# Optimization experiments

Measured on AMD Instinct MI355X. Metric: run time of the kernel, lower is better.

Reference implementation:

```python
import jax, jax.numpy as jnp
import numpy as np

NUM_EMBEDDINGS = 8192
EMBEDDING_DIM = 512
COMMITMENT_COST = 0.25


def setup_inputs() -> dict:
    key = jax.random.key(0)
    kz, ke = jax.random.split(key)
    z = jax.random.normal(kz, (2, EMBEDDING_DIM, 8, 32, 32), dtype=jnp.float32)
    # matches nn.Embedding init uniform_(-1/K, 1/K)
    emb_w = jax.random.uniform(
        ke, (NUM_EMBEDDINGS, EMBEDDING_DIM), dtype=jnp.float32,
        minval=-1.0 / NUM_EMBEDDINGS, maxval=1.0 / NUM_EMBEDDINGS)
    return {"z": z, "emb_w": emb_w}


def reference(z, emb_w):
    B, C, F, H, W = z.shape
    # [B,C,F,H,W] -> [N, C]
    z_flat = jnp.transpose(z, (0, 2, 3, 4, 1)).reshape(-1, C)
    # squared L2 distances via expansion: |z|^2 + |e|^2 - 2 z.e
    dist = (jnp.sum(z_flat * z_flat, axis=1, keepdims=True)
            + jnp.sum(emb_w * emb_w, axis=1)
            - 2.0 * jnp.matmul(z_flat, emb_w.T))  # [N, K]
    indices = jnp.argmin(dist, axis=1)  # [N]
    z_q_flat = emb_w[indices]  # [N, C]
    z_q = jnp.transpose(z_q_flat.reshape(B, F, H, W, C), (0, 4, 1, 2, 3))
    diff = z_q - z
    mse = jnp.mean(diff * diff)
    # codebook_loss == commitment_loss numerically (detach only affects grads)
    vq_loss = mse + COMMITMENT_COST * mse
    # straight-through estimator: value equals z_q
    z_q_ste = z + jax.lax.stop_gradient(z_q - z)
    indices = indices.reshape(B, F, H, W)
    return (z_q_ste, vq_loss, indices)
```

## Files before the change

### kernel.cpp

```cpp
#include <hip/hip_runtime.h>


constexpr int KCB = 8192;
constexpr int CD  = 512;
constexpr int SD  = 8192;
constexpr int NB  = 2;
constexpr int NR  = NB * SD;
constexpr long ZQ_ELEMS = (long)NB * CD * SD;

constexpr size_t WS_CNT   = 64;
constexpr size_t WS_KEYS  = 128;
constexpr size_t WS_RISK  = 139264;
constexpr size_t WS_IDX   = 212992;
constexpr size_t WS_LIST  = 286720;
constexpr size_t WS_ZNORM = 360448;
constexpr size_t WS_ENORM = 425984;
constexpr size_t WS_EMBT  = 458752;
constexpr size_t WS_ZH    = 17235968;
constexpr size_t WS_ZM    = 34013184;
constexpr size_t WS_EH    = 50790400;
constexpr size_t WS_EM    = 59179008;

#define RISK_EPS 2.0e-7f
#define WINDOW   1.3e-4f

constexpr int BUFB = 50176;

typedef __attribute__((ext_vector_type(8))) short short8;
typedef __attribute__((ext_vector_type(4))) float f32x4;

__device__ __forceinline__ unsigned int fkey(float f) {
  unsigned int b = __float_as_uint(f);
  return (b & 0x80000000u) ? ~b : (b | 0x80000000u);
}
__device__ __forceinline__ float unfkey(unsigned int u) {
  return (u & 0x80000000u) ? __uint_as_float(u ^ 0x80000000u)
                           : __uint_as_float(~u);
}
__device__ __forceinline__ ushort bf16_rne(float f, float* back) {
  unsigned int u = __float_as_uint(f);
  ushort h = (ushort)((u + 0x7FFFu + ((u >> 16) & 1u)) >> 16);
  *back = __uint_as_float((unsigned int)h << 16);
  return h;
}
__device__ __forceinline__ void gload16(const void* g, void* l) {
  __builtin_amdgcn_global_load_lds(
      (const __attribute__((address_space(1))) unsigned int*)g,
      (__attribute__((address_space(3))) unsigned int*)l, 16, 0, 0);
}

__global__ __launch_bounds__(256) void k_znorm(const float* __restrict__ z,
                                               float* __restrict__ znorm) {
  int n0 = blockIdx.x * 256;
  int b = n0 / SD, s0 = n0 % SD;
  const float* zp = z + (size_t)b * CD * SD + s0 + threadIdx.x;
  double a = 0.0;
  #pragma unroll 8
  for (int c = 0; c < CD; ++c) {
    double v = (double)zp[(size_t)c * SD];
    a = fma(v, v, a);
  }
  znorm[n0 + threadIdx.x] = (float)a;
}

__global__ __launch_bounds__(256) void k_enorm(const float* __restrict__ emb,
                                               float* __restrict__ enorm) {
  int row  = blockIdx.x * 4 + (threadIdx.x >> 6);
  int lane = threadIdx.x & 63;
  const float4* p = (const float4*)(emb + (size_t)row * CD);
  float4 a = p[lane * 2], b = p[lane * 2 + 1];
  float s = a.x*a.x + a.y*a.y + a.z*a.z + a.w*a.w
          + b.x*b.x + b.y*b.y + b.z*b.z + b.w*b.w;
  #pragma unroll
  for (int off = 32; off; off >>= 1) s += __shfl_down(s, off);
  if (lane == 0) enorm[row] = s;
}

__global__ __launch_bounds__(256) void k_transpose(const float* __restrict__ emb,
                                                   float* __restrict__ embt) {
  __shared__ float t[64][65];
  int bk = blockIdx.x & 127, bc = blockIdx.x >> 7;
  int k0 = bk * 64, c0 = bc * 64;
  int t4 = threadIdx.x & 15, tq = threadIdx.x >> 4;
  #pragma unroll
  for (int p = 0; p < 4; ++p) {
    int kk = p * 16 + tq;
    float4 v = *(const float4*)(emb + (size_t)(k0 + kk) * CD + c0 + 4 * t4);
    t[kk][4*t4+0] = v.x; t[kk][4*t4+1] = v.y; t[kk][4*t4+2] = v.z; t[kk][4*t4+3] = v.w;
  }
  __syncthreads();
  #pragma unroll
  for (int p = 0; p < 4; ++p) {
    int cc = p * 16 + tq;
    float4 v;
    v.x = t[4*t4+0][cc]; v.y = t[4*t4+1][cc]; v.z = t[4*t4+2][cc]; v.w = t[4*t4+3][cc];
    *(float4*)(embt + (size_t)(c0 + cc) * KCB + k0 + 4 * t4) = v;
  }
}


__global__ __launch_bounds__(256) void k_zsplit(const float* __restrict__ z,
                                                ushort* __restrict__ zh,
                                                ushort* __restrict__ zm) {
  __shared__ float t[32][257];
  int rt = blockIdx.x >> 4, ct = blockIdx.x & 15;
  int n0 = rt * 256;
  int b = n0 >> 13, s0 = n0 & (SD - 1);
  const float* zp = z + (size_t)b * CD * SD + (size_t)(ct * 32) * SD + s0;
  #pragma unroll 4
  for (int c = 0; c < 32; ++c)
    t[c][threadIdx.x] = zp[(size_t)c * SD + threadIdx.x];
  __syncthreads();
  size_t tbase = ((size_t)rt * 16 + ct) * 8192;
  #pragma unroll
  for (int p = 0; p < 4; ++p) {
    int slot = p * 256 + threadIdx.x;
    int r = slot >> 2, cs = slot & 3;
    int csw = cs ^ ((r >> 1) & 3);
    union { ushort u[8]; int4 v; } ph, pm;
    #pragma unroll
    for (int j = 0; j < 8; ++j) {
      float f = t[cs * 8 + j][r];
      float fh, fm;
      ph.u[j] = bf16_rne(f, &fh);
      float r1 = f - fh;
      pm.u[j] = bf16_rne(r1, &fm);
    }
    size_t off = tbase + (size_t)r * 32 + csw * 8;
    *(int4*)(zh + off) = ph.v;
    *(int4*)(zm + off) = pm.v;
  }
}

__global__ __launch_bounds__(256) void k_esplit(const float* __restrict__ emb,
                                                ushort* __restrict__ eh,
                                                ushort* __restrict__ em) {
  __shared__ float t[32][257];
  int rt = blockIdx.x >> 4, ct = blockIdx.x & 15;
  int k0 = rt * 256;
  #pragma unroll 4
  for (int i = 0; i < 32; ++i) {
    int idx = i * 256 + threadIdx.x;
    int r = idx >> 5, c = idx & 31;
    t[c][r] = emb[(size_t)(k0 + r) * CD + ct * 32 + c];
  }
  __syncthreads();
  size_t tbase = ((size_t)rt * 16 + ct) * 8192;
  #pragma unroll
  for (int p = 0; p < 4; ++p) {
    int slot = p * 256 + threadIdx.x;
    int r = slot >> 2, cs = slot & 3;
    int csw = cs ^ ((r >> 1) & 3);
    union { ushort u[8]; int4 v; } ph, pm;
    #pragma unroll
    for (int j = 0; j < 8; ++j) {
      float f = t[cs * 8 + j][r];
      float fh, fm;
      ph.u[j] = bf16_rne(f, &fh);
      float r1 = f - fh;
      pm.u[j] = bf16_rne(r1, &fm);
    }
    size_t off = tbase + (size_t)r * 32 + csw * 8;
    *(int4*)(eh + off) = ph.v;
    *(int4*)(em + off) = pm.v;
  }
}

__global__ __launch_bounds__(512, 2) void k_dist_mfma(
    const ushort* __restrict__ zh, const ushort* __restrict__ zm,
    const ushort* __restrict__ eh, const ushort* __restrict__ em,
    const float* __restrict__ enorm_g, const float* __restrict__ znorm,
    unsigned long long* __restrict__ keys, unsigned int* __restrict__ riskArr) {
  extern __shared__ __align__(16) char smem[];

  int tid  = threadIdx.x;
  int lane = tid & 63;
  int wid  = tid >> 6;
  int wm = wid >> 2, wn = wid & 3;
  int lk = lane >> 4, lc = lane & 15;

  int bid = (int)blockIdx.x;
  int swz = (bid & 7) * 32 + (bid >> 3);
  int m0    = (swz >> 1) * 128;
  int khalf = swz & 1;
  int n_rt  = m0 >> 8;
  int ahalf = (m0 >> 7) & 1;

  size_t thr8  = (size_t)tid * 8;
  int    tid16 = tid * 16;
  int    lane16 = lane * 16;

  int afo[4], bfo[4];
  #pragma unroll
  for (int mi = 0; mi < 4; ++mi) {
    int rowA = wm * 64 + mi * 16 + lc;
    afo[mi] = rowA * 64 + ((lk ^ ((rowA >> 1) & 3)) << 4);
  }
  #pragma unroll
  for (int ni = 0; ni < 4; ++ni) {
    int rowB = wn * 64 + ni * 16 + lc;
    bfo[ni] = rowB * 64 + ((lk ^ ((rowB >> 1) & 3)) << 4);
  }

  float Aab[16];
  #pragma unroll
  for (int li = 0; li < 16; ++li)
    Aab[li] = znorm[m0 + wm * 64 + (li >> 2) * 16 + lk * 4 + (li & 3)];

  unsigned long long bkey[16];
  float rminv[16];
  #pragma unroll
  for (int li = 0; li < 16; ++li) { bkey[li] = ~0ull; rminv[li] = 3.402823466e38f; }

#define STAGE(s_) do {                                                   \
    int it_ = (s_) >> 4, ks_ = (s_) & 15;                                \
    char* lb_ = smem + ((s_) % 3) * BUFB;                                \
    size_t ae_ = (size_t)(n_rt * 16 + ks_) * 8192 + (size_t)ahalf * 4096 \
                 + thr8;                                                 \
    size_t be_ = (size_t)((khalf * 16 + it_) * 16 + ks_) * 8192 + thr8;  \
    gload16(zh + ae_,        lb_ + tid16);                               \
    gload16(zm + ae_,        lb_ + 8192 + tid16);                        \
    gload16(eh + be_,        lb_ + 16384 + tid16);                       \
    gload16(eh + be_ + 4096, lb_ + 24576 + tid16);                       \
    gload16(em + be_,        lb_ + 32768 + tid16);                       \
    gload16(em + be_ + 4096, lb_ + 40960 + tid16);                       \
    gload16(enorm_g + (size_t)(khalf * 4096 + it_ * 256) + lane * 4,     \
            lb_ + 49152 + lane16);                                       \
  } while (0)

  STAGE(0);
  STAGE(1);

  for (int it = 0; it < 16; ++it) {
    f32x4 acc[4][4];
    #pragma unroll
    for (int mi = 0; mi < 4; ++mi)
      #pragma unroll
      for (int ni = 0; ni < 4; ++ni) {
        f32x4 zz = {0.f, 0.f, 0.f, 0.f};
        acc[mi][ni] = zz;
      }

    for (int ks = 0; ks < 16; ++ks) {
      int s = it * 16 + ks;
      if (s + 2 < 256) asm volatile("s_waitcnt vmcnt(7)" ::: "memory");
      else             asm volatile("s_waitcnt vmcnt(0)" ::: "memory");
      __builtin_amdgcn_s_barrier();
      __builtin_amdgcn_sched_barrier(0);
      if (s + 2 < 256) STAGE(s + 2);

      const char* Cb = smem + (s % 3) * BUFB;
      short8 a_h[4], a_m[4];
      #pragma unroll
      for (int mi = 0; mi < 4; ++mi) {
        a_h[mi] = *(const short8*)(Cb + afo[mi]);
        a_m[mi] = *(const short8*)(Cb + 8192 + afo[mi]);
      }
      #pragma unroll
      for (int ni = 0; ni < 4; ++ni) {
        short8 b_h = *(const short8*)(Cb + 16384 + bfo[ni]);
        short8 b_m = *(const short8*)(Cb + 32768 + bfo[ni]);
        #pragma unroll
        for (int mi = 0; mi < 4; ++mi)
          acc[mi][ni] = __builtin_amdgcn_mfma_f32_16x16x32_bf16(a_h[mi], b_h, acc[mi][ni], 0, 0, 0);
        #pragma unroll
        for (int mi = 0; mi < 4; ++mi)
          acc[mi][ni] = __builtin_amdgcn_mfma_f32_16x16x32_bf16(a_h[mi], b_m, acc[mi][ni], 0, 0, 0);
        #pragma unroll
        for (int mi = 0; mi < 4; ++mi)
          acc[mi][ni] = __builtin_amdgcn_mfma_f32_16x16x32_bf16(a_m[mi], b_h, acc[mi][ni], 0, 0, 0);
      }
    }

    int N0 = khalf * 4096 + it * 256;
    const char* Eb = smem + ((it * 16 + 15) % 3) * BUFB + 49152;
    #pragma unroll
    for (int ni = 0; ni < 4; ++ni) {
      int coff = wn * 64 + ni * 16 + lc;
      int col = N0 + coff;
      float en = *(const float*)(Eb + coff * 4);
      #pragma unroll
      for (int mi = 0; mi < 4; ++mi) {
        #pragma unroll
        for (int r = 0; r < 4; ++r) {
          int li = mi * 4 + r;
          float ab = Aab[li] + en;
          float q  = -2.0f * acc[mi][ni][r];
          float sv = ab + q;
          float bvv = sv - ab;
          float t   = q - bvv;
          unsigned int su = __float_as_uint(sv);
          float ulp = __uint_as_float(su & 0x7f800000u) * 1.1920929e-7f;
          bool risky = (0.5f * ulp - fabsf(t)) < RISK_EPS;
          if (((su & 0x7fffffu) == 0u) && (t < 0.f))
            risky |= ((0.25f * ulp + t) < RISK_EPS);
          unsigned long long key =
              ((unsigned long long)fkey(sv) << 32) | (unsigned int)col;
          if (key < bkey[li]) bkey[li] = key;
          if (risky && sv < rminv[li]) rminv[li] = sv;
        }
      }
    }
  }
#undef STAGE

  __syncthreads();
  unsigned long long* red = (unsigned long long*)smem;
  #pragma unroll
  for (int li = 0; li < 16; ++li) {
    int row = wm * 64 + (li >> 2) * 16 + lk * 4 + (li & 3);
    red[row * 64 + wn * 16 + lc] = bkey[li];
  }
  __syncthreads();
  if (tid < 128) {
    unsigned long long mn = ~0ull;
    #pragma unroll 4
    for (int i = 0; i < 64; ++i) {
      unsigned long long v = red[tid * 64 + i];
      if (v < mn) mn = v;
    }
    atomicMin(&keys[m0 + tid], mn);
  }
  __syncthreads();
  unsigned int* red2 = (unsigned int*)smem;
  #pragma unroll
  for (int li = 0; li < 16; ++li) {
    int row = wm * 64 + (li >> 2) * 16 + lk * 4 + (li & 3);
    red2[row * 64 + wn * 16 + lc] = fkey(rminv[li]);
  }
  __syncthreads();
  if (tid < 128) {
    unsigned int mn = 0xFFFFFFFFu;
    #pragma unroll 4
    for (int i = 0; i < 64; ++i) {
      unsigned int v = red2[tid * 64 + i];
      if (v < mn) mn = v;
    }
    atomicMin(&riskArr[m0 + tid], mn);
  }
}

__global__ __launch_bounds__(256) void k_resolve(const unsigned long long* __restrict__ keys,
                                                 const unsigned int* __restrict__ riskArr,
                                                 int* __restrict__ idxArr,
                                                 int* __restrict__ list,
                                                 unsigned int* __restrict__ cnt) {
  int row = blockIdx.x * 256 + threadIdx.x;
  unsigned long long kk = keys[row];
  idxArr[row] = (int)(kk & 0xffffffffull) & (KCB - 1);
  float smin = unfkey((unsigned int)(kk >> 32));
  float rmin = unfkey(riskArr[row]);
  if (rmin <= smin + WINDOW) {
    unsigned int pos = atomicAdd(cnt, 1u);
    list[pos & (NR - 1)] = row;
  }
}

__global__ __launch_bounds__(256) void k_rescan(const float* __restrict__ z,
                                                const float* __restrict__ embt,
                                                const float* __restrict__ enorm,
                                                const float* __restrict__ znorm,
                                                const int* __restrict__ list,
                                                const unsigned int* __restrict__ cnt,
                                                int* __restrict__ idxArr) {
  __shared__ float zs[512];
  __shared__ unsigned long long rk[256];
  int tid = threadIdx.x;
  unsigned int nr = *cnt;
  if (nr > (unsigned int)NR) nr = NR;
  for (unsigned int li = blockIdx.x; li < nr; li += gridDim.x) {
    int row = list[li] & (NR - 1);
    int b = row >> 13, s = row & (SD - 1);
    const float* zp = z + (size_t)b * CD * SD + s;
    zs[tid]       = zp[(size_t)tid * SD];
    zs[tid + 256] = zp[(size_t)(tid + 256) * SD];
    __syncthreads();
    float A = znorm[row];
    unsigned long long best = ~0ull;
    #pragma unroll 1
    for (int g = 0; g < 8; ++g) {
      int ka = tid + g * 1024;
      float a0 = 0.f, a1 = 0.f, a2 = 0.f, a3 = 0.f;
      #pragma unroll 8
      for (int c = 0; c < CD; ++c) {
        const float* ep = embt + (size_t)c * KCB + ka;
        float zc = zs[c];
        a0 = fmaf(zc, ep[0],   a0);
        a1 = fmaf(zc, ep[256], a1);
        a2 = fmaf(zc, ep[512], a2);
        a3 = fmaf(zc, ep[768], a3);
      }
      float av[4] = {a0, a1, a2, a3};
      #pragma unroll
      for (int jj = 0; jj < 4; ++jj) {
        int k = ka + jj * 256;
        float d = (A + enorm[k]) - 2.0f * av[jj];
        unsigned long long key =
            ((unsigned long long)fkey(d) << 32) | (unsigned int)k;
        if (key < best) best = key;
      }
    }
    rk[tid] = best;
    __syncthreads();
    for (int s2 = 128; s2; s2 >>= 1) {
      if (tid < s2 && rk[tid + s2] < rk[tid]) rk[tid] = rk[tid + s2];
      __syncthreads();
    }
    if (tid == 0) idxArr[row] = (int)(rk[0] & 0xffffffffull) & (KCB - 1);
    __syncthreads();
  }
}

__global__ __launch_bounds__(256) void k_gather(const float* __restrict__ z,
                                                const float* __restrict__ emb,
                                                const int* __restrict__ idxArr,
                                                float* __restrict__ out,
                                                double* __restrict__ acc) {
  __shared__ float q[64][129];
  __shared__ int   idxs[64];
  __shared__ float wpart[4];
  int tid = threadIdx.x;
  int n0 = blockIdx.x * 64;
  int b = n0 >> 13, s0 = n0 & (SD - 1);
  if (tid < 64) {
    int idx = idxArr[n0 + tid] & (KCB - 1);
    idxs[tid] = idx;
    out[ZQ_ELEMS + 1 + n0 + tid] = (float)idx;
  }
  __syncthreads();
  int sl = tid & 63;
  int cg = tid >> 6;
  float sum = 0.f;
  const float* zb = z   + (size_t)b * CD * SD + s0 + sl;
  float*       ob = out + (size_t)b * CD * SD + s0 + sl;
  for (int cc = 0; cc < 4; ++cc) {
    int cbase = cc * 128;
    __syncthreads();
    {
      int r = tid >> 2, p = tid & 3;
      const float* e = emb + (size_t)idxs[r] * CD + cbase + p * 32;
      #pragma unroll
      for (int j = 0; j < 8; ++j) {
        float4 v = *(const float4*)(e + j * 4);
        q[r][p*32 + j*4 + 0] = v.x; q[r][p*32 + j*4 + 1] = v.y;
        q[r][p*32 + j*4 + 2] = v.z; q[r][p*32 + j*4 + 3] = v.w;
      }
    }
    __syncthreads();
    #pragma unroll 8
    for (int j = 0; j < 32; ++j) {
      int c = cbase + cg * 32 + j;
      float zv = zb[(size_t)c * SD];
      float qv = q[sl][cg * 32 + j];
      float d = qv - zv;
      sum += d * d;
      ob[(size_t)c * SD] = zv + (qv - zv);
    }
  }
  #pragma unroll
  for (int off = 32; off; off >>= 1) sum += __shfl_down(sum, off);
  if ((tid & 63) == 0) wpart[tid >> 6] = sum;
  __syncthreads();
  if (tid == 0) {
    double t = (double)wpart[0] + (double)wpart[1] + (double)wpart[2] + (double)wpart[3];
    atomicAdd(acc, t);
  }
}

__global__ void k_loss(const double* __restrict__ acc, float* __restrict__ out) {
  out[ZQ_ELEMS] = (float)(1.25 * (*acc) / (double)ZQ_ELEMS);
}

extern "C" void kernel_launch(void* const* d_in, const int* in_sizes, int n_in,
                              void* d_out, int out_size, void* d_ws, size_t ws_size,
                              hipStream_t stream) {
  const float* z   = (const float*)d_in[0];
  const float* emb = (const float*)d_in[1];
  float* out = (float*)d_out;
  double*             acc   = (double*)d_ws;
  unsigned int*       cnt   = (unsigned int*)((char*)d_ws + WS_CNT);
  unsigned long long* keys  = (unsigned long long*)((char*)d_ws + WS_KEYS);
  unsigned int*       risk  = (unsigned int*)((char*)d_ws + WS_RISK);
  int*                idxA  = (int*)((char*)d_ws + WS_IDX);
  int*                list  = (int*)((char*)d_ws + WS_LIST);
  float*              znorm = (float*)((char*)d_ws + WS_ZNORM);
  float*              enorm = (float*)((char*)d_ws + WS_ENORM);
  float*              embt  = (float*)((char*)d_ws + WS_EMBT);
  ushort* zh = (ushort*)((char*)d_ws + WS_ZH);
  ushort* zm = (ushort*)((char*)d_ws + WS_ZM);
  ushort* eh = (ushort*)((char*)d_ws + WS_EH);
  ushort* em = (ushort*)((char*)d_ws + WS_EM);
  (void)in_sizes; (void)n_in; (void)out_size; (void)ws_size;

  hipMemsetAsync(d_ws, 0, 128, stream);
  hipMemsetAsync((char*)d_ws + WS_KEYS, 0xFF, (size_t)NR * 8, stream);
  hipMemsetAsync((char*)d_ws + WS_RISK, 0xFF, (size_t)NR * 4, stream);

  k_znorm    <<<NR / 256, 256, 0, stream>>>(z, znorm);
  k_enorm    <<<KCB / 4, 256, 0, stream>>>(emb, enorm);
  k_transpose<<<(KCB / 64) * (CD / 64), 256, 0, stream>>>(emb, embt);
  k_zsplit   <<<(NR / 256) * 16, 256, 0, stream>>>(z, zh, zm);
  k_esplit   <<<(KCB / 256) * 16, 256, 0, stream>>>(emb, eh, em);
  k_dist_mfma<<<256, 512, 3 * BUFB, stream>>>(zh, zm, eh, em,
                                              enorm, znorm, keys, risk);
  k_resolve  <<<NR / 256, 256, 0, stream>>>(keys, risk, idxA, list, cnt);
  k_rescan   <<<256, 256, 0, stream>>>(z, embt, enorm, znorm, list, cnt, idxA);
  k_gather   <<<NR / 64, 256, 0, stream>>>(z, emb, idxA, out, acc);
  k_loss     <<<1, 1, 0, stream>>>(acc, out);
}
```

Measured before the change: 685.9 us.

## Shrink distance-GEMM block tile to 128x128 with double-buffered 256-thread blocks

Reworks the MFMA distance kernel from 512-thread blocks with a 128x256 output tile and a three-stage LDS pipeline into 256-thread blocks with a 128x128 tile and a two-stage pipeline. The grid doubles to 512 blocks, with each block covering a quarter of the codebook. The intent is to improve occupancy and load balance and to cut the per-block LDS footprint. In exchange, each z tile is reloaded more often, the prefetch distance drops to one stage, and every k-step now needs a full __syncthreads. The cross-wave reduction width is halved to match the new tile.

```diff
diff --git a/kernel.cpp b/kernel.cpp
--- a/kernel.cpp
+++ b/kernel.cpp
@@ -24,7 +24,7 @@
 #define RISK_EPS 2.0e-7f
 #define WINDOW   1.3e-4f
 
-constexpr int BUFB = 50176;
+constexpr int BUFB = 33280;
 
 typedef __attribute__((ext_vector_type(8))) short short8;
 typedef __attribute__((ext_vector_type(4))) float f32x4;
@@ -166,7 +166,7 @@
   }
 }
 
-__global__ __launch_bounds__(512, 2) void k_dist_mfma(
+__global__ __launch_bounds__(256, 2) void k_dist_mfma(
     const ushort* __restrict__ zh, const ushort* __restrict__ zm,
     const ushort* __restrict__ eh, const ushort* __restrict__ em,
     const float* __restrict__ enorm_g, const float* __restrict__ znorm,
@@ -176,19 +176,19 @@
   int tid  = threadIdx.x;
   int lane = tid & 63;
   int wid  = tid >> 6;
-  int wm = wid >> 2, wn = wid & 3;
+  int wm = wid >> 1, wn = wid & 1;
   int lk = lane >> 4, lc = lane & 15;
 
   int bid = (int)blockIdx.x;
-  int swz = (bid & 7) * 32 + (bid >> 3);
-  int m0    = (swz >> 1) * 128;
-  int khalf = swz & 1;
+  int swz = (bid & 7) * 64 + (bid >> 3);
+  int mblk = swz >> 2;
+  int nq   = swz & 3;
+  int m0    = mblk * 128;
   int n_rt  = m0 >> 8;
   int ahalf = (m0 >> 7) & 1;
 
-  size_t thr8  = (size_t)tid * 8;
+  size_t thr8 = (size_t)tid * 8;
   int    tid16 = tid * 16;
-  int    lane16 = lane * 16;
 
   int afo[4], bfo[4];
   #pragma unroll
@@ -212,24 +212,27 @@
   #pragma unroll
   for (int li = 0; li < 16; ++li) { bkey[li] = ~0ull; rminv[li] = 3.402823466e38f; }
 
-#define STAGE(s_) do {                                                   \
-    int it_ = (s_) >> 4, ks_ = (s_) & 15;                                \
-    char* lb_ = smem + ((s_) % 3) * BUFB;                                \
-    size_t ae_ = (size_t)(n_rt * 16 + ks_) * 8192 + (size_t)ahalf * 4096 \
-                 + thr8;                                                 \
-    size_t be_ = (size_t)((khalf * 16 + it_) * 16 + ks_) * 8192 + thr8;  \
-    gload16(zh + ae_,        lb_ + tid16);                               \
-    gload16(zm + ae_,        lb_ + 8192 + tid16);                        \
-    gload16(eh + be_,        lb_ + 16384 + tid16);                       \
-    gload16(eh + be_ + 4096, lb_ + 24576 + tid16);                       \
-    gload16(em + be_,        lb_ + 32768 + tid16);                       \
-    gload16(em + be_ + 4096, lb_ + 40960 + tid16);                       \
-    gload16(enorm_g + (size_t)(khalf * 4096 + it_ * 256) + lane * 4,     \
-            lb_ + 49152 + lane16);                                       \
+#define STAGE(s_) do {                                                    \
+    int it_ = (s_) >> 4, ks_ = (s_) & 15;                                 \
+    char* lb_ = smem + ((s_) & 1) * BUFB;                                 \
+    size_t ae_ = (size_t)(n_rt * 16 + ks_) * 8192 + (size_t)ahalf * 4096  \
+                 + thr8;                                                  \
+    size_t be_ = (size_t)((nq * 8 + (it_ >> 1)) * 16 + ks_) * 8192        \
+                 + (size_t)(it_ & 1) * 4096 + thr8;                       \
+    gload16(zh + ae_,        lb_ + tid16);                                \
+    gload16(zh + ae_ + 2048, lb_ + 4096 + tid16);                         \
+    gload16(zm + ae_,        lb_ + 8192 + tid16);                         \
+    gload16(zm + ae_ + 2048, lb_ + 12288 + tid16);                        \
+    gload16(eh + be_,        lb_ + 16384 + tid16);                        \
+    gload16(eh + be_ + 2048, lb_ + 20480 + tid16);                        \
+    gload16(em + be_,        lb_ + 24576 + tid16);                        \
+    gload16(em + be_ + 2048, lb_ + 28672 + tid16);                        \
+    if (tid < 32)                                                         \
+      gload16(enorm_g + (size_t)(nq * 2048 + it_ * 128) + tid * 4,        \
+              lb_ + 32768 + tid16);                                      \
   } while (0)
 
   STAGE(0);
-  STAGE(1);
 
   for (int it = 0; it < 16; ++it) {
     f32x4 acc[4][4];
@@ -243,13 +246,10 @@
 
     for (int ks = 0; ks < 16; ++ks) {
       int s = it * 16 + ks;
-      if (s + 2 < 256) asm volatile("s_waitcnt vmcnt(7)" ::: "memory");
-      else             asm volatile("s_waitcnt vmcnt(0)" ::: "memory");
-      __builtin_amdgcn_s_barrier();
-      __builtin_amdgcn_sched_barrier(0);
-      if (s + 2 < 256) STAGE(s + 2);
-
-      const char* Cb = smem + (s % 3) * BUFB;
+      __syncthreads();
+      if (s + 1 < 256) STAGE(s + 1);
+
+      const char* Cb = smem + (s & 1) * BUFB;
       short8 a_h[4], a_m[4];
       #pragma unroll
       for (int mi = 0; mi < 4; ++mi) {
@@ -259,7 +259,7 @@
       #pragma unroll
       for (int ni = 0; ni < 4; ++ni) {
         short8 b_h = *(const short8*)(Cb + 16384 + bfo[ni]);
-        short8 b_m = *(const short8*)(Cb + 32768 + bfo[ni]);
+        short8 b_m = *(const short8*)(Cb + 24576 + bfo[ni]);
         #pragma unroll
         for (int mi = 0; mi < 4; ++mi)
           acc[mi][ni] = __builtin_amdgcn_mfma_f32_16x16x32_bf16(a_h[mi], b_h, acc[mi][ni], 0, 0, 0);
@@ -272,8 +272,8 @@
       }
     }
 
-    int N0 = khalf * 4096 + it * 256;
-    const char* Eb = smem + ((it * 16 + 15) % 3) * BUFB + 49152;
+    int N0 = nq * 2048 + it * 128;
+    const char* Eb = smem + BUFB + 32768;
     #pragma unroll
     for (int ni = 0; ni < 4; ++ni) {
       int coff = wn * 64 + ni * 16 + lc;
@@ -309,14 +309,14 @@
   #pragma unroll
   for (int li = 0; li < 16; ++li) {
     int row = wm * 64 + (li >> 2) * 16 + lk * 4 + (li & 3);
-    red[row * 64 + wn * 16 + lc] = bkey[li];
+    red[row * 32 + wn * 16 + lc] = bkey[li];
   }
   __syncthreads();
   if (tid < 128) {
     unsigned long long mn = ~0ull;
     #pragma unroll 4
-    for (int i = 0; i < 64; ++i) {
-      unsigned long long v = red[tid * 64 + i];
+    for (int i = 0; i < 32; ++i) {
+      unsigned long long v = red[tid * 32 + i];
       if (v < mn) mn = v;
     }
     atomicMin(&keys[m0 + tid], mn);
@@ -326,14 +326,14 @@
   #pragma unroll
   for (int li = 0; li < 16; ++li) {
     int row = wm * 64 + (li >> 2) * 16 + lk * 4 + (li & 3);
-    red2[row * 64 + wn * 16 + lc] = fkey(rminv[li]);
+    red2[row * 32 + wn * 16 + lc] = fkey(rminv[li]);
   }
   __syncthreads();
   if (tid < 128) {
     unsigned int mn = 0xFFFFFFFFu;
     #pragma unroll 4
-    for (int i = 0; i < 64; ++i) {
-      unsigned int v = red2[tid * 64 + i];
+    for (int i = 0; i < 32; ++i) {
+      unsigned int v = red2[tid * 32 + i];
       if (v < mn) mn = v;
     }
     atomicMin(&riskArr[m0 + tid], mn);
@@ -501,7 +501,7 @@
   k_transpose<<<(KCB / 64) * (CD / 64), 256, 0, stream>>>(emb, embt);
   k_zsplit   <<<(NR / 256) * 16, 256, 0, stream>>>(z, zh, zm);
   k_esplit   <<<(KCB / 256) * 16, 256, 0, stream>>>(emb, eh, em);
-  k_dist_mfma<<<256, 512, 3 * BUFB, stream>>>(zh, zm, eh, em,
+  k_dist_mfma<<<512, 256, 2 * BUFB, stream>>>(zh, zm, eh, em,
                                               enorm, znorm, keys, risk);
   k_resolve  <<<NR / 256, 256, 0, stream>>>(keys, risk, idxA, list, cnt);
   k_rescan   <<<256, 256, 0, stream>>>(z, embt, enorm, znorm, list, cnt, idxA);
```

Measured after the change: 685.6 us. Within noise of the previous version (-0.1%).
